# Optimization experiments

Hardware: AMD Instinct MI355X
Metric: run time of the kernel (lower is better)

Reference implementation:

```python
import jax, jax.numpy as jnp
import numpy as np
import math

B, T, INP_DIM, OUT_DIM = 2, 4096, 1, 64
DEPTH, D_MODEL, N_HEADS, D_FF = 4, 512, 8, 2048
D_HEAD = D_MODEL // N_HEADS
EPS = 1e-5


def setup_inputs() -> dict:
    key = jax.random.key(0)
    ks = jax.random.split(key, 16)
    s = 0.02
    inp = {
        "x_in": jax.random.normal(ks[0], (B, T, INP_DIM), dtype=jnp.float32),
        "inp_w": jax.random.normal(ks[1], (INP_DIM, D_MODEL), dtype=jnp.float32) * s,
        "inp_b": jnp.zeros((D_MODEL,), dtype=jnp.float32),
        "pos_emb": jax.random.normal(ks[2], (T, D_MODEL), dtype=jnp.float32) * s,
        "ln1_g": jnp.ones((DEPTH, D_MODEL), dtype=jnp.float32),
        "ln1_b": jnp.zeros((DEPTH, D_MODEL), dtype=jnp.float32),
        "qkv_w": jax.random.normal(ks[3], (DEPTH, D_MODEL, 3 * D_MODEL), dtype=jnp.float32) * s,
        "proj_w": jax.random.normal(ks[4], (DEPTH, D_MODEL, D_MODEL), dtype=jnp.float32) * s,
        "ln2_g": jnp.ones((DEPTH, D_MODEL), dtype=jnp.float32),
        "ln2_b": jnp.zeros((DEPTH, D_MODEL), dtype=jnp.float32),
        "fc1_w": jax.random.normal(ks[5], (DEPTH, D_MODEL, D_FF), dtype=jnp.float32) * s,
        "fc2_w": jax.random.normal(ks[6], (DEPTH, D_FF, D_MODEL), dtype=jnp.float32) * s,
        "lnf_g": jnp.ones((D_MODEL,), dtype=jnp.float32),
        "lnf_b": jnp.zeros((D_MODEL,), dtype=jnp.float32),
        "head_w": jax.random.normal(ks[7], (D_MODEL, OUT_DIM), dtype=jnp.float32) * s,
        "head_b": jnp.zeros((OUT_DIM,), dtype=jnp.float32),
    }
    return inp


def _layernorm(x, g, b):
    mu = jnp.mean(x, axis=-1, keepdims=True)
    var = jnp.mean(jnp.square(x - mu), axis=-1, keepdims=True)
    return (x - mu) * jax.lax.rsqrt(var + EPS) * g + b


def _attn(x, qkv_w, proj_w):
    Bx, Tx, d = x.shape
    qkv = x @ qkv_w  # [B,T,3d]
    q, k, v = jnp.split(qkv, 3, axis=-1)
    q = q.reshape(Bx, Tx, N_HEADS, D_HEAD)
    k = k.reshape(Bx, Tx, N_HEADS, D_HEAD)
    v = v.reshape(Bx, Tx, N_HEADS, D_HEAD)
    scores = jnp.einsum('bqhd,bkhd->bhqk', q, k) / math.sqrt(D_HEAD)
    causal = jnp.tril(jnp.ones((Tx, Tx), dtype=bool))
    scores = jnp.where(causal, scores, -jnp.inf)
    attn = jax.nn.softmax(scores, axis=-1)
    out = jnp.einsum('bhqk,bkhd->bqhd', attn, v).reshape(Bx, Tx, d)
    return out @ proj_w


def reference(x_in, inp_w, inp_b, pos_emb, ln1_g, ln1_b, qkv_w, proj_w,
              ln2_g, ln2_b, fc1_w, fc2_w, lnf_g, lnf_b, head_w, head_b):
    x = x_in @ inp_w + inp_b + pos_emb[None, :, :]  # [B,T,d]
    for l in range(DEPTH):
        x = x + _attn(_layernorm(x, ln1_g[l], ln1_b[l]), qkv_w[l], proj_w[l])
        h = _layernorm(x, ln2_g[l], ln2_b[l])
        h = jax.nn.gelu(h @ fc1_w[l], approximate=False) @ fc2_w[l]
        x = x + h
    h = _layernorm(x, lnf_g, lnf_b)
    return h @ head_w + head_b  # [B,T,out_dim]
```

## Files before the change

### kernel.cpp

```cpp
#include <hip/hip_runtime.h>
#include <math.h>

typedef unsigned short u16;
typedef unsigned int u32;

#define B_ 2
#define T_ 4096
#define DM 512
#define NH 8
#define DH 64
#define DFF 2048
#define MTOT (B_*T_)

#define SCALEQ 0.18033688011112042f

using f32x4  = __attribute__((ext_vector_type(4))) float;
using f32x16 = __attribute__((ext_vector_type(16))) float;
using bf16x8 = __attribute__((ext_vector_type(8))) short;

__device__ __forceinline__ float b2f(u16 u) {
  union { u32 u; float f; } v; v.u = ((u32)u) << 16; return v.f;
}
__device__ __forceinline__ u16 f2b(float f) {
  union { float f; u32 u; } v; v.f = f;
  u32 r = v.u + 0x7FFFu + ((v.u >> 16) & 1u);
  return (u16)(r >> 16);
}
__device__ __forceinline__ u32 cvtpk(float lo, float hi) {
  u32 r;
  asm("v_cvt_pk_bf16_f32 %0, %1, %2" : "=v"(r) : "v"(lo), "v"(hi));
  return r;
}
#if __has_builtin(__builtin_amdgcn_exp2f)
#define EXP2(x) __builtin_amdgcn_exp2f(x)
#else
#define EXP2(x) __expf((x) * 0.6931471805599453f)
#endif
#if __has_builtin(__builtin_amdgcn_rcpf)
#define RCP(x) __builtin_amdgcn_rcpf(x)
#else
#define RCP(x) (1.0f / (x))
#endif

__device__ __forceinline__ void gload_lds(const u16* g, u16* l) {
  __builtin_amdgcn_global_load_lds(
      (const __attribute__((address_space(1))) void*)g,
      (__attribute__((address_space(3))) void*)l, 16, 0, 0);
}

__device__ __forceinline__ int lsw(int row, int col) {
  int slot = ((col >> 3) + (row >> 3) + 2 * (row & 7)) & 7;
  return (row << 6) + (slot << 3) + (col & 7);
}

__global__ __launch_bounds__(256) void embed_k(
    const float* __restrict__ x_in, const float* __restrict__ w,
    const float* __restrict__ bias, const float* __restrict__ pos,
    float* __restrict__ x) {
  int idx = blockIdx.x * 256 + threadIdx.x;
  int row = idx >> 9, d = idx & 511;
  int t = row & (T_ - 1);
  x[idx] = x_in[row] * w[d] + bias[d] + pos[t * DM + d];
}

template<int NP>
__global__ __launch_bounds__(256) void ln_k(
    float* __restrict__ x, const float* __restrict__ P,
    const float* __restrict__ g, const float* __restrict__ bet,
    u16* __restrict__ y) {
  int wid = threadIdx.x >> 6, lane = threadIdx.x & 63;
  int row = blockIdx.x * 4 + wid;
  float* xr = x + (size_t)row * DM + lane * 8;
  float4 a0 = *(const float4*)xr;
  float4 a1 = *(const float4*)(xr + 4);
  float v[8] = {a0.x, a0.y, a0.z, a0.w, a1.x, a1.y, a1.z, a1.w};
  if (NP > 0) {
#pragma unroll
    for (int s = 0; s < NP; s++) {
      const float* pr = P + (size_t)s * MTOT * DM + (size_t)row * DM + lane * 8;
      float4 p0 = *(const float4*)pr;
      float4 p1 = *(const float4*)(pr + 4);
      v[0] += p0.x; v[1] += p0.y; v[2] += p0.z; v[3] += p0.w;
      v[4] += p1.x; v[5] += p1.y; v[6] += p1.z; v[7] += p1.w;
    }
    float4 w0; w0.x = v[0]; w0.y = v[1]; w0.z = v[2]; w0.w = v[3];
    float4 w1; w1.x = v[4]; w1.y = v[5]; w1.z = v[6]; w1.w = v[7];
    *(float4*)xr = w0;
    *(float4*)(xr + 4) = w1;
  }
  float s = 0.f;
#pragma unroll
  for (int j = 0; j < 8; j++) s += v[j];
#pragma unroll
  for (int off = 32; off; off >>= 1) s += __shfl_xor(s, off);
  float mu = s * (1.0f / DM);
  float q = 0.f;
#pragma unroll
  for (int j = 0; j < 8; j++) { float e = v[j] - mu; q += e * e; }
#pragma unroll
  for (int off = 32; off; off >>= 1) q += __shfl_xor(q, off);
  float rs = rsqrtf(q * (1.0f / DM) + 1e-5f);
  float4 g0 = *(const float4*)(g + lane * 8);
  float4 g1 = *(const float4*)(g + lane * 8 + 4);
  float4 p0 = *(const float4*)(bet + lane * 8);
  float4 p1 = *(const float4*)(bet + lane * 8 + 4);
  float gg[8] = {g0.x, g0.y, g0.z, g0.w, g1.x, g1.y, g1.z, g1.w};
  float pp[8] = {p0.x, p0.y, p0.z, p0.w, p1.x, p1.y, p1.z, p1.w};
  uint4 st;
  st.x = cvtpk((v[0]-mu)*rs*gg[0]+pp[0], (v[1]-mu)*rs*gg[1]+pp[1]);
  st.y = cvtpk((v[2]-mu)*rs*gg[2]+pp[2], (v[3]-mu)*rs*gg[3]+pp[3]);
  st.z = cvtpk((v[4]-mu)*rs*gg[4]+pp[4], (v[5]-mu)*rs*gg[5]+pp[5]);
  st.w = cvtpk((v[6]-mu)*rs*gg[6]+pp[6], (v[7]-mu)*rs*gg[7]+pp[7]);
  *(uint4*)(y + (size_t)row * DM + lane * 8) = st;
}

__global__ __launch_bounds__(256) void wconv_k(
    const float* __restrict__ W, u16* __restrict__ Wt, int K, int N) {
  __shared__ float tile[32][33];
  const float* Wl = W + (size_t)blockIdx.z * K * N;
  u16* Wtl = Wt + (size_t)blockIdx.z * K * N;
  int k0 = blockIdx.x * 32, n0 = blockIdx.y * 32;
  int r = threadIdx.x >> 3, c4 = (threadIdx.x & 7) * 4;
  *(float4*)&tile[r][c4] = *(const float4*)(Wl + (size_t)(k0 + r) * N + n0 + c4);
  __syncthreads();
  uint2 st;
  st.x = cvtpk(tile[c4 + 0][r], tile[c4 + 1][r]);
  st.y = cvtpk(tile[c4 + 2][r], tile[c4 + 3][r]);
  *(uint2*)(Wtl + (size_t)(n0 + r) * K + k0 + c4) = st;
}

template<int EPI>
__global__ __launch_bounds__(256) void gemm_k(
    const u16* __restrict__ A, const u16* __restrict__ Bt,
    u16* __restrict__ Cb, float* __restrict__ Cf,
    int M, int N, int K, int Kslice, int scale_cols) {
  __shared__ u16 As[2][128][32];
  __shared__ u16 Bs[2][128][32];
  int tid = threadIdx.x;
  int lane = tid & 63, wid = tid >> 6;
  int wr = wid >> 1, wc = wid & 1;
  int m0 = blockIdx.y * 128, n0 = blockIdx.x * 128;
  int kbeg = blockIdx.z * Kslice;
  if (EPI == 3) Cf += (size_t)blockIdx.z * M * N;
  f32x4 acc[4][4] = {};
  int rsub = lane >> 2, ksub = (lane & 3) * 8;
  const u16* Ab = A  + (size_t)(m0 + wid * 32 + rsub) * K + kbeg + ksub;
  const u16* Bb = Bt + (size_t)(n0 + wid * 32 + rsub) * K + kbeg + ksub;
#define GSTAGE(BUF, KO) { \
    gload_lds(Ab + (KO), &As[BUF][wid * 32][0]); \
    gload_lds(Ab + (size_t)16 * K + (KO), &As[BUF][wid * 32 + 16][0]); \
    gload_lds(Bb + (KO), &Bs[BUF][wid * 32][0]); \
    gload_lds(Bb + (size_t)16 * K + (KO), &Bs[BUF][wid * 32 + 16][0]); }
  GSTAGE(0, 0);
  __syncthreads();
  int r = lane & 15, kc = (lane >> 4) * 8;
  for (int k0 = 0; k0 < Kslice; k0 += 32) {
    int cur = (k0 >> 5) & 1;
    if (k0 + 32 < Kslice) GSTAGE(cur ^ 1, k0 + 32);
    bf16x8 af[4], bfr[4];
#pragma unroll
    for (int m = 0; m < 4; m++) af[m]  = *(const bf16x8*)&As[cur][wr*64 + m*16 + r][kc];
#pragma unroll
    for (int n = 0; n < 4; n++) bfr[n] = *(const bf16x8*)&Bs[cur][wc*64 + n*16 + r][kc];
#pragma unroll
    for (int m = 0; m < 4; m++)
#pragma unroll
      for (int n = 0; n < 4; n++)
        acc[m][n] = __builtin_amdgcn_mfma_f32_16x16x32_bf16(af[m], bfr[n], acc[m][n], 0, 0, 0);
    __syncthreads();
  }
  int r4 = (lane >> 4) * 4, cN = lane & 15;
#pragma unroll
  for (int m = 0; m < 4; m++) {
#pragma unroll
    for (int n = 0; n < 4; n++) {
      int col = n0 + wc*64 + n*16 + cN;
#pragma unroll
      for (int i = 0; i < 4; i++) {
        int row = m0 + wr*64 + m*16 + r4 + i;
        size_t off = (size_t)row * N + col;
        float v = acc[m][n][i];
        if (EPI == 0) {
          if (col < scale_cols) v *= SCALEQ;
          Cb[off] = f2b(v);
        } else if (EPI == 1) {
          Cf[off] += v;
        } else if (EPI == 3) {
          Cf[off] = v;
        } else {
          float e = EXP2(v * (2.3022082f + 0.10294324f * v * v));
          Cb[off] = f2b(v * (1.0f - RCP(e + 1.0f)));
        }
      }
    }
  }
}

__global__ __launch_bounds__(256) void attn_k(const u16* __restrict__ qkv,
                                              u16* __restrict__ Opart,
                                              float* __restrict__ ml) {
  __shared__ u16 Ks[2][64 * 64];
  __shared__ u16 Vt[2][64 * 64];
  int tid = threadIdx.x;
  int w = tid >> 6, l = tid & 63;
  int hh = l >> 5, c = l & 31;
  int flat = blockIdx.y * 144 + blockIdx.x;
  int swz = (flat & 7) * 288 + (flat >> 3);
  int bh = swz / 144, slot = swz - bh * 144;
  int g = 0;
  while (2 * (g + 1) * (g + 2) <= slot) g++;
  int s2 = slot - 2 * g * (g + 1);
  int qb = 4 * g + s2 / (g + 1);
  int ck = s2 - (s2 / (g + 1)) * (g + 1);
  int ntot = 2 * qb + 2;
  int kt0 = ck * 8;
  int kt1 = kt0 + 8 < ntot ? kt0 + 8 : ntot;
  int b = bh >> 3, hd = bh & 7;
  int q0w = qb * 128 + w * 32;
  int q_abs = q0w + c;
  size_t base = (size_t)b * T_ * 1536;
  bf16x8 qf[4];
  const u16* qp = qkv + base + (size_t)q_abs * 1536 + hd * 64 + hh * 8;
#pragma unroll
  for (int kk = 0; kk < 4; kk++) qf[kk] = *(const bf16x8*)(qp + kk * 16);
  f32x16 oa0 = {}, oa1 = {};
  float m_run = -1e30f, l_run = 0.f;
  int sp = tid >> 3, d8 = (tid & 7) * 8;
  int r0 = sp * 2, r1 = r0 + 1;
  const u16* kvbase = qkv + base + DM + hd * 64 + d8;
  uint4 kreg0, kreg1, vreg0, vreg1;
#define AGLOAD(KT) { \
    const u16* s0_ = kvbase + (size_t)((KT) * 64 + r0) * 1536; \
    kreg0 = *(const uint4*)s0_; vreg0 = *(const uint4*)(s0_ + DM); \
    const u16* s1_ = s0_ + 1536; \
    kreg1 = *(const uint4*)s1_; vreg1 = *(const uint4*)(s1_ + DM); }
  AGLOAD(kt0);
  for (int kt = kt0; kt < kt1; kt++) {
    u16* Kb = Ks[kt & 1];
    u16* Vb = Vt[kt & 1];
    *(uint4*)&Kb[lsw(r0, d8)] = kreg0;
    *(uint4*)&Kb[lsw(r1, d8)] = kreg1;
    {
      const u16* v0 = (const u16*)&vreg0;
      const u16* v1 = (const u16*)&vreg1;
#pragma unroll
      for (int j = 0; j < 8; j++) {
        u32 pw = (u32)v0[j] | ((u32)v1[j] << 16);
        *(u32*)&Vb[lsw(d8 + j, r0)] = pw;
      }
    }
    if (kt + 1 < kt1) AGLOAD(kt + 1);
    __syncthreads();
    if (kt * 64 > q0w + 31) continue;
    bool needMask = (kt * 64 + 63 > q0w);
    f32x16 sa0 = {}, sa1 = {};
    __builtin_amdgcn_s_setprio(1);
#pragma unroll
    for (int kk = 0; kk < 4; kk++) {
      bf16x8 ka  = *(const bf16x8*)&Kb[lsw(c,      kk * 16 + hh * 8)];
      bf16x8 kb2 = *(const bf16x8*)&Kb[lsw(32 + c, kk * 16 + hh * 8)];
      sa0 = __builtin_amdgcn_mfma_f32_32x32x16_bf16(ka,  qf[kk], sa0, 0, 0, 0);
      sa1 = __builtin_amdgcn_mfma_f32_32x32x16_bf16(kb2, qf[kk], sa1, 0, 0, 0);
    }
    __builtin_amdgcn_s_setprio(0);
    if (needMask) {
#pragma unroll
      for (int gi = 0; gi < 4; gi++)
#pragma unroll
        for (int i = 0; i < 4; i++) {
          int krow = kt * 64 + gi * 8 + hh * 4 + i;
          if (krow > q_abs)      sa0[gi * 4 + i] = -1e30f;
          if (krow + 32 > q_abs) sa1[gi * 4 + i] = -1e30f;
        }
    }
    float pm = -1e30f;
#pragma unroll
    for (int r = 0; r < 16; r++) pm = fmaxf(pm, fmaxf(sa0[r], sa1[r]));
    pm = fmaxf(pm, __shfl_xor(pm, 32));
    if (!__all(pm - m_run <= 8.0f)) {
      float mnew = fmaxf(m_run, pm);
      float corr = EXP2(m_run - mnew);
      l_run *= corr;
#pragma unroll
      for (int r = 0; r < 16; r++) { oa0[r] *= corr; oa1[r] *= corr; }
      m_run = mnew;
    }
    float lsum = 0.f;
#pragma unroll
    for (int r = 0; r < 16; r++) {
      float e0 = EXP2(sa0[r] - m_run); sa0[r] = e0;
      float e1 = EXP2(sa1[r] - m_run); sa1[r] = e1;
      lsum += e0 + e1;
    }
    lsum += __shfl_xor(lsum, 32);
    l_run += lsum;
    u32 Aw[8], Bw_[8], Asw[8], Bsw[8];
#pragma unroll
    for (int r2 = 0; r2 < 4; r2++) {
      Aw[r2]      = cvtpk(sa0[4 * r2 + 0], sa0[4 * r2 + 1]);
      Bw_[r2]     = cvtpk(sa0[4 * r2 + 2], sa0[4 * r2 + 3]);
      Aw[4 + r2]  = cvtpk(sa1[4 * r2 + 0], sa1[4 * r2 + 1]);
      Bw_[4 + r2] = cvtpk(sa1[4 * r2 + 2], sa1[4 * r2 + 3]);
    }
#pragma unroll
    for (int i = 0; i < 8; i++) {
      Asw[i] = __shfl_xor(Aw[i], 32);
      Bsw[i] = __shfl_xor(Bw_[i], 32);
    }
    __builtin_amdgcn_s_setprio(1);
#pragma unroll
    for (int ks = 0; ks < 4; ks++) {
      int mo = (ks >> 1) * 4;
      int r2e = mo + 2 * (ks & 1), r2o = r2e + 1;
      union { u32 wd[4]; bf16x8 v; } u;
      u.wd[0] = hh ? Asw[r2o] : Aw[r2e];
      u.wd[1] = hh ? Bsw[r2o] : Bw_[r2e];
      u.wd[2] = hh ? Aw[r2o]  : Asw[r2e];
      u.wd[3] = hh ? Bw_[r2o] : Bsw[r2e];
      bf16x8 va = *(const bf16x8*)&Vb[lsw(c,      ks * 16 + hh * 8)];
      bf16x8 vb = *(const bf16x8*)&Vb[lsw(32 + c, ks * 16 + hh * 8)];
      oa0 = __builtin_amdgcn_mfma_f32_32x32x16_bf16(va, u.v, oa0, 0, 0, 0);
      oa1 = __builtin_amdgcn_mfma_f32_32x32x16_bf16(vb, u.v, oa1, 0, 0, 0);
    }
    __builtin_amdgcn_s_setprio(0);
  }
  int sidx = bh * 144 + slot;
  u16* op = Opart + ((size_t)sidx * 128 + w * 32 + c) * 64;
#pragma unroll
  for (int gi = 0; gi < 4; gi++) {
    uint2 s0, s1;
    s0.x = cvtpk(oa0[4*gi+0], oa0[4*gi+1]);
    s0.y = cvtpk(oa0[4*gi+2], oa0[4*gi+3]);
    s1.x = cvtpk(oa1[4*gi+0], oa1[4*gi+1]);
    s1.y = cvtpk(oa1[4*gi+2], oa1[4*gi+3]);
    int d0 = gi * 8 + hh * 4;
    *(uint2*)(op + d0)      = s0;
    *(uint2*)(op + 32 + d0) = s1;
  }
  if (hh == 0) {
    float2 p; p.x = m_run; p.y = l_run;
    *(float2*)&ml[((size_t)sidx * 128 + w * 32 + c) * 2] = p;
  }
}

__global__ __launch_bounds__(256) void comb_k(
    const u16* __restrict__ Opart, const float* __restrict__ ml,
    u16* __restrict__ attno) {
  int gi = blockIdx.x * 256 + threadIdx.x;
  int d = gi & 63, bhq = gi >> 6;
  int bh = bhq >> 12, q = bhq & 4095;
  int qb = q >> 7, ri = q & 127;
  int g = qb >> 2;
  int nc = g + 1;
  int bs = 2 * g * (g + 1) + (qb & 3) * (g + 1);
  int s0 = bh * 144 + bs;
  float M = -1e30f;
  for (int cc = 0; cc < nc; cc++)
    M = fmaxf(M, ml[((size_t)(s0 + cc) * 128 + ri) * 2]);
  float O = 0.f, L = 0.f;
  for (int cc = 0; cc < nc; cc++) {
    float2 p = *(const float2*)&ml[((size_t)(s0 + cc) * 128 + ri) * 2];
    float wgt = EXP2(p.x - M);
    L += p.y * wgt;
    O += b2f(Opart[((size_t)(s0 + cc) * 128 + ri) * 64 + d]) * wgt;
  }
  int b = bh >> 3, hd = bh & 7;
  attno[((size_t)b * T_ + q) * DM + hd * 64 + d] = f2b(O / L);
}

__global__ __launch_bounds__(256) void head_k(
    const u16* __restrict__ xb, const float* __restrict__ W,
    const float* __restrict__ bias, float* __restrict__ out) {
  int wid = threadIdx.x >> 6, lane = threadIdx.x & 63;
  int row = blockIdx.x * 4 + wid;
  const u16* xr = xb + (size_t)row * DM;
  float a0 = 0.f, a1 = 0.f, a2 = 0.f, a3 = 0.f;
  for (int d = 0; d < DM; d += 8) {
    uint4 xv = *(const uint4*)(xr + d);
    const u16* xp = (const u16*)&xv;
    const float* Wp = W + (size_t)d * 64 + lane;
    a0 += b2f(xp[0]) * Wp[0];
    a1 += b2f(xp[1]) * Wp[64];
    a2 += b2f(xp[2]) * Wp[128];
    a3 += b2f(xp[3]) * Wp[192];
    a0 += b2f(xp[4]) * Wp[256];
    a1 += b2f(xp[5]) * Wp[320];
    a2 += b2f(xp[6]) * Wp[384];
    a3 += b2f(xp[7]) * Wp[448];
  }
  out[(size_t)row * 64 + lane] = a0 + a1 + a2 + a3 + bias[lane];
}

extern "C" void kernel_launch(void* const* d_in, const int* in_sizes, int n_in,
                              void* d_out, int out_size, void* d_ws, size_t ws_size,
                              hipStream_t stream) {
  (void)in_sizes; (void)n_in; (void)out_size; (void)ws_size;
  const float* x_in  = (const float*)d_in[0];
  const float* inp_w = (const float*)d_in[1];
  const float* inp_b = (const float*)d_in[2];
  const float* pos   = (const float*)d_in[3];
  const float* ln1g  = (const float*)d_in[4];
  const float* ln1b  = (const float*)d_in[5];
  const float* qkvw  = (const float*)d_in[6];
  const float* projw = (const float*)d_in[7];
  const float* ln2g  = (const float*)d_in[8];
  const float* ln2b  = (const float*)d_in[9];
  const float* fc1w  = (const float*)d_in[10];
  const float* fc2w  = (const float*)d_in[11];
  const float* lnfg  = (const float*)d_in[12];
  const float* lnfb  = (const float*)d_in[13];
  const float* headw = (const float*)d_in[14];
  const float* headb = (const float*)d_in[15];

  char* ws = (char*)d_ws;
  size_t off = 0;
  float* x     = (float*)(ws + off); off += (size_t)MTOT * DM * 4;
  u16*  lnb    = (u16*)(ws + off);   off += (size_t)MTOT * DM * 2;
  u16*  qkvb   = (u16*)(ws + off);   off += (size_t)MTOT * 3 * DM * 2;
  u16*  attno  = (u16*)(ws + off);   off += (size_t)MTOT * DM * 2;
  u16*  ff     = qkvb;
  u16*  qkvt   = (u16*)(ws + off);   off += (size_t)4 * DM * 3 * DM * 2;
  u16*  projt  = (u16*)(ws + off);   off += (size_t)4 * DM * DM * 2;
  u16*  fc1t   = (u16*)(ws + off);   off += (size_t)4 * DM * DFF * 2;
  u16*  fc2t   = (u16*)(ws + off);   off += (size_t)4 * DFF * DM * 2;
  char* shared = ws + off;
  u16*  Opart  = (u16*)shared;
  float* mlbuf = (float*)(shared + (size_t)16 * 144 * 128 * 64 * 2);
  float* fcp   = (float*)shared;

  wconv_k<<<dim3(16, 48, 4), 256, 0, stream>>>(qkvw,  qkvt, DM, 3 * DM);
  wconv_k<<<dim3(16, 16, 4), 256, 0, stream>>>(projw, projt, DM, DM);
  wconv_k<<<dim3(16, 64, 4), 256, 0, stream>>>(fc1w,  fc1t, DM, DFF);
  wconv_k<<<dim3(64, 16, 4), 256, 0, stream>>>(fc2w,  fc2t, DFF, DM);

  embed_k<<<(MTOT * DM) / 256, 256, 0, stream>>>(x_in, inp_w, inp_b, pos, x);
  for (int ly = 0; ly < 4; ly++) {
    if (ly == 0)
      ln_k<0><<<MTOT / 4, 256, 0, stream>>>(x, nullptr, ln1g, ln1b, lnb);
    else
      ln_k<2><<<MTOT / 4, 256, 0, stream>>>(x, fcp, ln1g + ly * DM, ln1b + ly * DM, lnb);
    gemm_k<0><<<dim3(12, 64), 256, 0, stream>>>(lnb, qkvt + (size_t)ly * DM * 3 * DM,
                                                qkvb, nullptr, MTOT, 3 * DM, DM, DM, DM);
    attn_k<<<dim3(144, 16), 256, 0, stream>>>(qkvb, Opart, mlbuf);
    comb_k<<<(16 * 4096 * 64) / 256, 256, 0, stream>>>(Opart, mlbuf, attno);
    gemm_k<1><<<dim3(4, 64), 256, 0, stream>>>(attno, projt + (size_t)ly * DM * DM,
                                               nullptr, x, MTOT, DM, DM, DM, 0);
    ln_k<0><<<MTOT / 4, 256, 0, stream>>>(x, nullptr, ln2g + ly * DM, ln2b + ly * DM, lnb);
    gemm_k<2><<<dim3(16, 64), 256, 0, stream>>>(lnb, fc1t + (size_t)ly * DM * DFF,
                                                ff, nullptr, MTOT, DFF, DM, DM, 0);
    gemm_k<3><<<dim3(4, 64, 2), 256, 0, stream>>>(ff, fc2t + (size_t)ly * DFF * DM,
                                                  nullptr, fcp, MTOT, DM, DFF, DFF / 2, 0);
  }
  ln_k<2><<<MTOT / 4, 256, 0, stream>>>(x, fcp, lnfg, lnfb, lnb);
  head_k<<<MTOT / 4, 256, 0, stream>>>(lnb, headw, headb, (float*)d_out);
}
```

Measured before the change: 1.025 ms.

## Use direct-to-LDS K loads, permlane swaps, vectorized combine, split-K proj GEMM

The attention kernel drops K/V double buffering, loads K straight into LDS with swizzled source columns, and replaces the 16 cross-half shuffles with permlane32_swap. It also sets an occupancy hint of 5 blocks and turns the max and sum reductions into trees. The combine kernel handles 4 head dims per thread with vector loads and stores. The output projection now uses the split-K GEMM that writes to fcp, with the residual add folded into the following layernorm. The aim is to cut LDS, shuffle and launch overhead, at the cost of a second barrier per tile and no K prefetch overlap.

```diff
diff --git a/kernel.cpp b/kernel.cpp
--- a/kernel.cpp
+++ b/kernel.cpp
@@ -17,6 +17,7 @@
 using f32x4  = __attribute__((ext_vector_type(4))) float;
 using f32x16 = __attribute__((ext_vector_type(16))) float;
 using bf16x8 = __attribute__((ext_vector_type(8))) short;
+typedef unsigned int u32x2 __attribute__((ext_vector_type(2)));
 
 __device__ __forceinline__ float b2f(u16 u) {
   union { u32 u; float f; } v; v.u = ((u32)u) << 16; return v.f;
@@ -196,11 +197,21 @@
   }
 }
 
-__global__ __launch_bounds__(256) void attn_k(const u16* __restrict__ qkv,
-                                              u16* __restrict__ Opart,
-                                              float* __restrict__ ml) {
-  __shared__ u16 Ks[2][64 * 64];
-  __shared__ u16 Vt[2][64 * 64];
+#if __has_builtin(__builtin_amdgcn_permlane32_swap)
+#define PLSWAP(A, B, O0, O1) { \
+    u32x2 r_ = __builtin_amdgcn_permlane32_swap((A), (B), false, false); \
+    O0 = r_.x; O1 = r_.y; }
+#else
+#define PLSWAP(A, B, O0, O1) { \
+    u32 as_ = __shfl_xor((u32)(A), 32), bs_ = __shfl_xor((u32)(B), 32); \
+    O0 = hh ? bs_ : (A); O1 = hh ? (B) : as_; }
+#endif
+
+__global__ __launch_bounds__(256, 5) void attn_k(const u16* __restrict__ qkv,
+                                                 u16* __restrict__ Opart,
+                                                 float* __restrict__ ml) {
+  __shared__ u16 Ks[64 * 64];
+  __shared__ u16 Vt[64 * 64];
   int tid = threadIdx.x;
   int w = tid >> 6, l = tid & 63;
   int hh = l >> 5, c = l & 31;
@@ -225,40 +236,49 @@
   for (int kk = 0; kk < 4; kk++) qf[kk] = *(const bf16x8*)(qp + kk * 16);
   f32x16 oa0 = {}, oa1 = {};
   float m_run = -1e30f, l_run = 0.f;
+  const u16* kvb = qkv + base + DM + hd * 64;
+  int lr = l >> 3, ls = l & 7;
+  int rA = w * 8 + lr;
+  int rB = (w + 4) * 8 + lr;
+  int cA = ((ls - w - 2 * (rA & 7)) & 7) * 8;
+  int cB = ((ls - (w + 4) - 2 * (rB & 7)) & 7) * 8;
+  const u16* ksrcA = kvb + (size_t)rA * 1536 + cA;
+  const u16* ksrcB = kvb + (size_t)rB * 1536 + cB;
+  u16* kdstA = &Ks[w * 512];
+  u16* kdstB = &Ks[(w + 4) * 512];
   int sp = tid >> 3, d8 = (tid & 7) * 8;
   int r0 = sp * 2, r1 = r0 + 1;
-  const u16* kvbase = qkv + base + DM + hd * 64 + d8;
-  uint4 kreg0, kreg1, vreg0, vreg1;
-#define AGLOAD(KT) { \
-    const u16* s0_ = kvbase + (size_t)((KT) * 64 + r0) * 1536; \
-    kreg0 = *(const uint4*)s0_; vreg0 = *(const uint4*)(s0_ + DM); \
-    const u16* s1_ = s0_ + 1536; \
-    kreg1 = *(const uint4*)s1_; vreg1 = *(const uint4*)(s1_ + DM); }
-  AGLOAD(kt0);
+  uint4 vreg0, vreg1;
+#define AGV(KT) { \
+    const u16* s_ = kvb + DM + (size_t)((KT) * 64 + r0) * 1536 + d8; \
+    vreg0 = *(const uint4*)s_; vreg1 = *(const uint4*)(s_ + 1536); }
+  AGV(kt0);
   for (int kt = kt0; kt < kt1; kt++) {
-    u16* Kb = Ks[kt & 1];
-    u16* Vb = Vt[kt & 1];
-    *(uint4*)&Kb[lsw(r0, d8)] = kreg0;
-    *(uint4*)&Kb[lsw(r1, d8)] = kreg1;
+    __syncthreads();
+    {
+      size_t ko = (size_t)kt * 64 * 1536;
+      gload_lds(ksrcA + ko, kdstA);
+      gload_lds(ksrcB + ko, kdstB);
+    }
     {
       const u16* v0 = (const u16*)&vreg0;
       const u16* v1 = (const u16*)&vreg1;
 #pragma unroll
       for (int j = 0; j < 8; j++) {
         u32 pw = (u32)v0[j] | ((u32)v1[j] << 16);
-        *(u32*)&Vb[lsw(d8 + j, r0)] = pw;
+        *(u32*)&Vt[lsw(d8 + j, r0)] = pw;
       }
     }
-    if (kt + 1 < kt1) AGLOAD(kt + 1);
     __syncthreads();
+    if (kt + 1 < kt1) AGV(kt + 1);
     if (kt * 64 > q0w + 31) continue;
     bool needMask = (kt * 64 + 63 > q0w);
     f32x16 sa0 = {}, sa1 = {};
     __builtin_amdgcn_s_setprio(1);
 #pragma unroll
     for (int kk = 0; kk < 4; kk++) {
-      bf16x8 ka  = *(const bf16x8*)&Kb[lsw(c,      kk * 16 + hh * 8)];
-      bf16x8 kb2 = *(const bf16x8*)&Kb[lsw(32 + c, kk * 16 + hh * 8)];
+      bf16x8 ka  = *(const bf16x8*)&Ks[lsw(c,      kk * 16 + hh * 8)];
+      bf16x8 kb2 = *(const bf16x8*)&Ks[lsw(32 + c, kk * 16 + hh * 8)];
       sa0 = __builtin_amdgcn_mfma_f32_32x32x16_bf16(ka,  qf[kk], sa0, 0, 0, 0);
       sa1 = __builtin_amdgcn_mfma_f32_32x32x16_bf16(kb2, qf[kk], sa1, 0, 0, 0);
     }
@@ -273,9 +293,12 @@
           if (krow + 32 > q_abs) sa1[gi * 4 + i] = -1e30f;
         }
     }
-    float pm = -1e30f;
-#pragma unroll
-    for (int r = 0; r < 16; r++) pm = fmaxf(pm, fmaxf(sa0[r], sa1[r]));
+    float t[8];
+#pragma unroll
+    for (int r = 0; r < 8; r++)
+      t[r] = fmaxf(fmaxf(sa0[r], sa0[r + 8]), fmaxf(sa1[r], sa1[r + 8]));
+    float pm = fmaxf(fmaxf(fmaxf(t[0], t[1]), fmaxf(t[2], t[3])),
+                     fmaxf(fmaxf(t[4], t[5]), fmaxf(t[6], t[7])));
     pm = fmaxf(pm, __shfl_xor(pm, 32));
     if (!__all(pm - m_run <= 8.0f)) {
       float mnew = fmaxf(m_run, pm);
@@ -285,16 +308,21 @@
       for (int r = 0; r < 16; r++) { oa0[r] *= corr; oa1[r] *= corr; }
       m_run = mnew;
     }
-    float lsum = 0.f;
+    float sarr[16];
 #pragma unroll
     for (int r = 0; r < 16; r++) {
       float e0 = EXP2(sa0[r] - m_run); sa0[r] = e0;
       float e1 = EXP2(sa1[r] - m_run); sa1[r] = e1;
-      lsum += e0 + e1;
-    }
+      sarr[r] = e0 + e1;
+    }
+#pragma unroll
+    for (int r = 0; r < 8; r++) sarr[r] += sarr[r + 8];
+#pragma unroll
+    for (int r = 0; r < 4; r++) sarr[r] += sarr[r + 4];
+    float lsum = (sarr[0] + sarr[1]) + (sarr[2] + sarr[3]);
     lsum += __shfl_xor(lsum, 32);
     l_run += lsum;
-    u32 Aw[8], Bw_[8], Asw[8], Bsw[8];
+    u32 Aw[8], Bw_[8];
 #pragma unroll
     for (int r2 = 0; r2 < 4; r2++) {
       Aw[r2]      = cvtpk(sa0[4 * r2 + 0], sa0[4 * r2 + 1]);
@@ -302,23 +330,16 @@
       Aw[4 + r2]  = cvtpk(sa1[4 * r2 + 0], sa1[4 * r2 + 1]);
       Bw_[4 + r2] = cvtpk(sa1[4 * r2 + 2], sa1[4 * r2 + 3]);
     }
-#pragma unroll
-    for (int i = 0; i < 8; i++) {
-      Asw[i] = __shfl_xor(Aw[i], 32);
-      Bsw[i] = __shfl_xor(Bw_[i], 32);
-    }
     __builtin_amdgcn_s_setprio(1);
 #pragma unroll
     for (int ks = 0; ks < 4; ks++) {
       int mo = (ks >> 1) * 4;
       int r2e = mo + 2 * (ks & 1), r2o = r2e + 1;
       union { u32 wd[4]; bf16x8 v; } u;
-      u.wd[0] = hh ? Asw[r2o] : Aw[r2e];
-      u.wd[1] = hh ? Bsw[r2o] : Bw_[r2e];
-      u.wd[2] = hh ? Aw[r2o]  : Asw[r2e];
-      u.wd[3] = hh ? Bw_[r2o] : Bsw[r2e];
-      bf16x8 va = *(const bf16x8*)&Vb[lsw(c,      ks * 16 + hh * 8)];
-      bf16x8 vb = *(const bf16x8*)&Vb[lsw(32 + c, ks * 16 + hh * 8)];
+      PLSWAP(Aw[r2e], Aw[r2o], u.wd[0], u.wd[2]);
+      PLSWAP(Bw_[r2e], Bw_[r2o], u.wd[1], u.wd[3]);
+      bf16x8 va = *(const bf16x8*)&Vt[lsw(c,      ks * 16 + hh * 8)];
+      bf16x8 vb = *(const bf16x8*)&Vt[lsw(32 + c, ks * 16 + hh * 8)];
       oa0 = __builtin_amdgcn_mfma_f32_32x32x16_bf16(va, u.v, oa0, 0, 0, 0);
       oa1 = __builtin_amdgcn_mfma_f32_32x32x16_bf16(vb, u.v, oa1, 0, 0, 0);
     }
@@ -347,7 +368,8 @@
     const u16* __restrict__ Opart, const float* __restrict__ ml,
     u16* __restrict__ attno) {
   int gi = blockIdx.x * 256 + threadIdx.x;
-  int d = gi & 63, bhq = gi >> 6;
+  int d4 = (gi & 15) * 4;
+  int bhq = gi >> 4;
   int bh = bhq >> 12, q = bhq & 4095;
   int qb = q >> 7, ri = q & 127;
   int g = qb >> 2;
@@ -357,15 +379,22 @@
   float M = -1e30f;
   for (int cc = 0; cc < nc; cc++)
     M = fmaxf(M, ml[((size_t)(s0 + cc) * 128 + ri) * 2]);
-  float O = 0.f, L = 0.f;
+  float O0 = 0.f, O1 = 0.f, O2 = 0.f, O3 = 0.f, L = 0.f;
   for (int cc = 0; cc < nc; cc++) {
     float2 p = *(const float2*)&ml[((size_t)(s0 + cc) * 128 + ri) * 2];
     float wgt = EXP2(p.x - M);
     L += p.y * wgt;
-    O += b2f(Opart[((size_t)(s0 + cc) * 128 + ri) * 64 + d]) * wgt;
-  }
+    uint2 ov = *(const uint2*)&Opart[((size_t)(s0 + cc) * 128 + ri) * 64 + d4];
+    const u16* opx = (const u16*)&ov;
+    O0 += b2f(opx[0]) * wgt; O1 += b2f(opx[1]) * wgt;
+    O2 += b2f(opx[2]) * wgt; O3 += b2f(opx[3]) * wgt;
+  }
+  float invL = 1.0f / L;
   int b = bh >> 3, hd = bh & 7;
-  attno[((size_t)b * T_ + q) * DM + hd * 64 + d] = f2b(O / L);
+  uint2 st;
+  st.x = cvtpk(O0 * invL, O1 * invL);
+  st.y = cvtpk(O2 * invL, O3 * invL);
+  *(uint2*)&attno[((size_t)b * T_ + q) * DM + hd * 64 + d4] = st;
 }
 
 __global__ __launch_bounds__(256) void head_k(
@@ -442,10 +471,10 @@
     gemm_k<0><<<dim3(12, 64), 256, 0, stream>>>(lnb, qkvt + (size_t)ly * DM * 3 * DM,
                                                 qkvb, nullptr, MTOT, 3 * DM, DM, DM, DM);
     attn_k<<<dim3(144, 16), 256, 0, stream>>>(qkvb, Opart, mlbuf);
-    comb_k<<<(16 * 4096 * 64) / 256, 256, 0, stream>>>(Opart, mlbuf, attno);
-    gemm_k<1><<<dim3(4, 64), 256, 0, stream>>>(attno, projt + (size_t)ly * DM * DM,
-                                               nullptr, x, MTOT, DM, DM, DM, 0);
-    ln_k<0><<<MTOT / 4, 256, 0, stream>>>(x, nullptr, ln2g + ly * DM, ln2b + ly * DM, lnb);
+    comb_k<<<(16 * 4096 * 16) / 256, 256, 0, stream>>>(Opart, mlbuf, attno);
+    gemm_k<3><<<dim3(4, 64, 2), 256, 0, stream>>>(attno, projt + (size_t)ly * DM * DM,
+                                                  nullptr, fcp, MTOT, DM, DM, DM / 2, 0);
+    ln_k<2><<<MTOT / 4, 256, 0, stream>>>(x, fcp, ln2g + ly * DM, ln2b + ly * DM, lnb);
     gemm_k<2><<<dim3(16, 64), 256, 0, stream>>>(lnb, fc1t + (size_t)ly * DM * DFF,
                                                 ff, nullptr, MTOT, DFF, DM, DM, 0);
     gemm_k<3><<<dim3(4, 64, 2), 256, 0, stream>>>(ff, fc2t + (size_t)ly * DFF * DM,
```

New measurement: 1.263 ms. +23.2%, slower.
